# Kernel optimization log

Hardware: AMD Instinct MI355X
Metric: run time of the kernel (lower is better)

## Reference

```python
import jax, jax.numpy as jnp
import numpy as np

B, N, D = 4, 160, 64
ZI, ZE, L, LE = 64, 64, 4, 8
H1, H2 = 128, 64


def setup_inputs() -> dict:
    key = jax.random.key(0)
    ks = jax.random.split(key, 20)
    s = 0.05
    inp = {
        "node_embeddings": jax.random.normal(ks[0], (B, N, D), jnp.float32),
        "z_intra_t": jax.random.normal(ks[1], (B, ZI), jnp.float32),
        "z_inter_t": jax.random.normal(ks[2], (B, ZE), jnp.float32),
        # lag embedding table
        "lag_emb": jax.random.normal(ks[3], (L, LE), jnp.float32),
        # instantaneous reasoner: (2D+ZI)->128->64->1
        "Wi1": jax.random.normal(ks[4], (2 * D + ZI, H1), jnp.float32) * s,
        "bi1": jnp.zeros((H1,), jnp.float32),
        "Wi2": jax.random.normal(ks[5], (H1, H2), jnp.float32) * s,
        "bi2": jnp.zeros((H2,), jnp.float32),
        "Wi3": jax.random.normal(ks[6], (H2, 1), jnp.float32) * s,
        "bi3": jnp.zeros((1,), jnp.float32),
        # lagged reasoner: (2D+ZE+LE)->128->64->1
        "Wl1": jax.random.normal(ks[7], (2 * D + ZE + LE, H1), jnp.float32) * s,
        "bl1": jnp.zeros((H1,), jnp.float32),
        "Wl2": jax.random.normal(ks[8], (H1, H2), jnp.float32) * s,
        "bl2": jnp.zeros((H2,), jnp.float32),
        "Wl3": jax.random.normal(ks[9], (H2, 1), jnp.float32) * s,
        "bl3": jnp.zeros((1,), jnp.float32),
    }
    return inp


def reference(node_embeddings, z_intra_t, z_inter_t, lag_emb,
              Wi1, bi1, Wi2, bi2, Wi3, bi3,
              Wl1, bl1, Wl2, bl2, Wl3, bl3):
    # Instead of materializing concat([h_i, h_j, z, ...]) over N*N pairs,
    # split the first linear layer's weight along its input rows; the sum of
    # per-part projections equals the linear over the concatenation.
    ne = node_embeddings  # [B, N, D]

    # --- instantaneous reasoner ---
    Wi1_a, Wi1_b, Wi1_z = Wi1[:D], Wi1[D:2 * D], Wi1[2 * D:]
    pi = ne @ Wi1_a          # [B, N, H1] projection of h_i
    pj = ne @ Wi1_b          # [B, N, H1] projection of h_j
    pz = z_intra_t @ Wi1_z   # [B, H1]
    h = jax.nn.relu(pi[:, :, None, :] + pj[:, None, :, :]
                    + pz[:, None, None, :] + bi1)          # [B, N, N, H1]
    h = jax.nn.relu(h @ Wi2 + bi2)                         # [B, N, N, H2]
    W_logits = (h @ Wi3 + bi3)[..., 0]                     # [B, N, N]

    # --- lagged reasoner ---
    Wl1_a, Wl1_b = Wl1[:D], Wl1[D:2 * D]
    Wl1_z, Wl1_l = Wl1[2 * D:2 * D + ZE], Wl1[2 * D + ZE:]
    qi = ne @ Wl1_a          # [B, N, H1]
    qj = ne @ Wl1_b          # [B, N, H1]
    qz = z_inter_t @ Wl1_z   # [B, H1]
    ql = lag_emb @ Wl1_l     # [L, H1]
    g = jax.nn.relu(qi[:, None, :, None, :] + qj[:, None, None, :, :]
                    + qz[:, None, None, None, :] + ql[None, :, None, None, :]
                    + bl1)                                 # [B, L, N, N, H1]
    g = jax.nn.relu(g @ Wl2 + bl2)                         # [B, L, N, N, H2]
    A_logits = (g @ Wl3 + bl3)[..., 0]                     # [B, L, N, N]

    mask = 1.0 - jnp.eye(N, dtype=ne.dtype)
    W_t = jax.nn.sigmoid(W_logits) * mask
    A_lags_t = jax.nn.sigmoid(A_logits) * mask
    return (W_t, A_lags_t)
```

## Files before the change

### kernel.cpp

```cpp
#include <hip/hip_runtime.h>
#include <hip/hip_bf16.h>

#define B_   4
#define N_   160
#define D_   64
#define ZI_  64
#define H1_  128
#define H2_  64
#define L_   4
#define LE_  8

typedef __bf16 bf16x8 __attribute__((ext_vector_type(8)));
typedef float  f32x4  __attribute__((ext_vector_type(4)));
typedef unsigned int u32x4 __attribute__((ext_vector_type(4)));

static __device__ __forceinline__ unsigned pk_bf16(float a, float b) {
    __hip_bfloat162 h = __float22bfloat162_rn(float2{a, b});
    union { __hip_bfloat162 h; unsigned u; } c;
    c.h = h;
    return c.u;
}

__global__ __launch_bounds__(128) void stage_a(
    const float* __restrict__ ne,
    const float* __restrict__ zi,
    const float* __restrict__ ze,
    const float* __restrict__ lag,
    const float* __restrict__ Wi1,
    const float* __restrict__ bi1,
    const float* __restrict__ Wl1,
    const float* __restrict__ bl1,
    const float* __restrict__ Wi2,
    const float* __restrict__ bi2,
    const float* __restrict__ Wi3,
    const float* __restrict__ bi3,
    const float* __restrict__ Wl2,
    const float* __restrict__ bl2,
    const float* __restrict__ Wl3,
    const float* __restrict__ bl3,
    float* __restrict__ ui, float* __restrict__ uq,
    __bf16* __restrict__ vpi, __bf16* __restrict__ vpl,
    char* __restrict__ blob_i, char* __restrict__ blob_l)
{
    const int bi = blockIdx.x;
    const int b  = bi / N_;
    const int h  = threadIdx.x;

    const float* nerow = ne + bi * D_;

    float pi_ = 0.f, pj_ = 0.f, qi_ = 0.f, qj_ = 0.f;
#pragma unroll 16
    for (int d = 0; d < D_; ++d) {
        const float a = nerow[d];
        pi_ += a * Wi1[d * H1_ + h];
        pj_ += a * Wi1[(D_ + d) * H1_ + h];
        qi_ += a * Wl1[d * H1_ + h];
        qj_ += a * Wl1[(D_ + d) * H1_ + h];
    }
    float pz = 0.f, qz = 0.f;
#pragma unroll 16
    for (int z = 0; z < ZI_; ++z) {
        pz += zi[b * ZI_ + z] * Wi1[(2 * D_ + z) * H1_ + h];
        qz += ze[b * ZI_ + z] * Wl1[(2 * D_ + z) * H1_ + h];
    }

    ui[bi * H1_ + h] = pi_ + pz + bi1[h];

    const int hsw = (((h >> 3) ^ (bi & 7)) << 3) | (h & 7);
    vpi[bi * H1_ + hsw] = (__bf16)pj_;
    vpl[bi * H1_ + hsw] = (__bf16)qj_;

    const float qbase = qi_ + qz + bl1[h];
#pragma unroll
    for (int l = 0; l < L_; ++l) {
        float ql = 0.f;
#pragma unroll
        for (int e = 0; e < LE_; ++e)
            ql += lag[l * LE_ + e] * Wl1[(2 * D_ + ZI_ + e) * H1_ + h];
        uq[((b * L_ + l) * N_ + (bi % N_)) * H1_ + h] = qbase + ql;
    }

    if (bi < 2) {
        const float* Wsrc = (bi == 0) ? Wi2 : Wl2;
        char* blob = (bi == 0) ? blob_i : blob_l;
        __bf16* Wdst = (__bf16*)blob;
#pragma unroll
        for (int r = 0; r < 8; ++r) {
            const int fc = h + 128 * r;
            const int kt = fc >> 8, ct = (fc >> 6) & 3;
            const int q = (fc >> 4) & 3, c = fc & 15;
            bf16x8 t;
#pragma unroll
            for (int j = 0; j < 8; ++j)
                t[j] = (__bf16)Wsrc[(32 * kt + 8 * q + j) * H2_ + 16 * ct + c];
            *(bf16x8*)(Wdst + fc * 8) = t;
        }
        float* bdst = (float*)(blob + 16384);
        const float* b2s = (bi == 0) ? bi2 : bl2;
        const float* w3s = (bi == 0) ? Wi3 : Wl3;
        const float* b3s = (bi == 0) ? bi3 : bl3;
        if (h < H2_) bdst[h] = b2s[h];
        if (h < H2_) bdst[128 + h] = w3s[h];
        if (h == 0)  bdst[256] = b3s[0];
    }
}

__global__ __launch_bounds__(256, 3) void stage_b(
    const float* __restrict__ ui, const float* __restrict__ uq,
    const __bf16* __restrict__ vpi, const __bf16* __restrict__ vpl,
    const char* __restrict__ blob_i, const char* __restrict__ blob_l,
    float* __restrict__ out)
{
    __shared__ __align__(16) char lds[43008];
    __bf16* panel = (__bf16*)lds;
    char*   blob  = lds + 20480;
    float*  ulds  = (float*)(lds + 40960);

    const int t    = threadIdx.x;
    const int wid  = t >> 6;
    const int lane = t & 63;
    const int q = lane >> 4;
    const int c = lane & 15;

    const int blk    = blockIdx.x;
    const int rowgrp = blk >> 1;
    const int half   = blk & 1;
    const int wave   = rowgrp * 4 + wid;
    const int wave0  = rowgrp * 4;

    const __bf16* psrc;
    const char*   bsrc;
    const float*  usrc;
    if (rowgrp < 160) {
        psrc = vpi + (rowgrp / 40) * (N_ * H1_);
        bsrc = blob_i;
        usrc = ui + wave0 * H1_;
    } else {
        psrc = vpl + ((rowgrp - 160) / 160) * (N_ * H1_);
        bsrc = blob_l;
        usrc = uq + (wave0 - B_ * N_) * H1_;
    }
    psrc += 80 * half * H1_;

    {
        const char* gp = (const char*)psrc;
#pragma unroll
        for (int it = 0; it < 5; ++it)
            __builtin_amdgcn_global_load_lds(
                (const __attribute__((address_space(1))) void*)(gp + it * 4096 + t * 16),
                (__attribute__((address_space(3))) void*)(lds + it * 4096 + wid * 1024),
                16, 0, 0);
#pragma unroll
        for (int it = 0; it < 5; ++it)
            __builtin_amdgcn_global_load_lds(
                (const __attribute__((address_space(1))) void*)(bsrc + it * 4096 + t * 16),
                (__attribute__((address_space(3))) void*)(blob + it * 4096 + wid * 1024),
                16, 0, 0);
        if (wid < 2)
            __builtin_amdgcn_global_load_lds(
                (const __attribute__((address_space(1))) void*)((const char*)usrc + t * 16),
                (__attribute__((address_space(3))) void*)((char*)ulds + wid * 1024),
                16, 0, 0);
    }

    long obase;
    int  i;
    if (wave < B_ * N_) {
        i = wave % N_;
        obase = (long)wave * N_;
    } else {
        const int w2i = wave - B_ * N_;
        i = w2i % N_;
        obase = (long)B_ * N_ * N_ + (long)w2i * N_;
    }

    __syncthreads();

    bf16x8 bfr[4][4];
#pragma unroll
    for (int kt = 0; kt < 4; ++kt)
#pragma unroll
        for (int ct = 0; ct < 4; ++ct)
            bfr[kt][ct] = *(const bf16x8*)(blob + ((kt * 4 + ct) * 64 + lane) * 16);

    const float* bf32 = (const float*)(blob + 16384);
    float b2c[4], w3c[4];
#pragma unroll
    for (int ct = 0; ct < 4; ++ct) {
        b2c[ct] = bf32[16 * ct + c];
        w3c[ct] = bf32[128 + 16 * ct + c];
    }
    const float b3f = bf32[256];

    const float* ubase = ulds + wid * H1_;
    f32x4 ue[4], uo[4];
#pragma unroll
    for (int kt = 0; kt < 4; ++kt) {
        const f32x4 a0 = *(const f32x4*)(ubase + 32 * kt + 8 * q);
        const f32x4 a1 = *(const f32x4*)(ubase + 32 * kt + 8 * q + 4);
        ue[kt] = (f32x4){a0[0], a0[2], a1[0], a1[2]};
        uo[kt] = (f32x4){a0[1], a0[3], a1[1], a1[3]};
    }

    for (int jt = 0; jt < 5; ++jt) {
        const __bf16* prow = panel + (16 * jt + c) * H1_;
        f32x4 acc[4];
#pragma unroll
        for (int ct = 0; ct < 4; ++ct)
            acc[ct] = (f32x4){b2c[ct], b2c[ct], b2c[ct], b2c[ct]};

#pragma unroll
        for (int kt = 0; kt < 4; ++kt) {
            const u32x4 vw = *(const u32x4*)(prow + (((4 * kt + q) ^ (c & 7)) << 3));
            f32x4 vlo, vhi;
#pragma unroll
            for (int d = 0; d < 4; ++d) {
                vlo[d] = __uint_as_float(vw[d] << 16);
                vhi[d] = __uint_as_float(vw[d] & 0xffff0000u);
            }
            f32x4 xe = ue[kt] + vlo;
            f32x4 xo = uo[kt] + vhi;
            xe = __builtin_elementwise_max(xe, (f32x4)0.f);
            xo = __builtin_elementwise_max(xo, (f32x4)0.f);
            union { bf16x8 v; unsigned d[4]; } a;
#pragma unroll
            for (int d = 0; d < 4; ++d)
                a.d[d] = pk_bf16(xe[d], xo[d]);
#pragma unroll
            for (int ct = 0; ct < 4; ++ct)
                acc[ct] = __builtin_amdgcn_mfma_f32_16x16x32_bf16(
                    a.v, bfr[kt][ct], acc[ct], 0, 0, 0);
        }

        float logit[4];
#pragma unroll
        for (int r = 0; r < 4; ++r) {
            float p = 0.f;
#pragma unroll
            for (int ct = 0; ct < 4; ++ct)
                p += fmaxf(acc[ct][r], 0.f) * w3c[ct];
            p += __shfl_xor(p, 1);
            p += __shfl_xor(p, 2);
            p += __shfl_xor(p, 4);
            p += __shfl_xor(p, 8);
            logit[r] = p;
        }

        if (c < 4) {
            const int j = 80 * half + 16 * jt + 4 * q + c;
            const float lg = logit[c] + b3f;
            const float s = (j == i) ? 0.f : 1.f / (1.f + __expf(-lg));
            out[obase + j] = s;
        }
    }
}

extern "C" void kernel_launch(void* const* d_in, const int* in_sizes, int n_in,
                              void* d_out, int out_size, void* d_ws, size_t ws_size,
                              hipStream_t stream) {
    const float* ne  = (const float*)d_in[0];
    const float* zi  = (const float*)d_in[1];
    const float* ze  = (const float*)d_in[2];
    const float* lag = (const float*)d_in[3];
    const float* Wi1 = (const float*)d_in[4];
    const float* bi1 = (const float*)d_in[5];
    const float* Wi2 = (const float*)d_in[6];
    const float* bi2 = (const float*)d_in[7];
    const float* Wi3 = (const float*)d_in[8];
    const float* bi3 = (const float*)d_in[9];
    const float* Wl1 = (const float*)d_in[10];
    const float* bl1 = (const float*)d_in[11];
    const float* Wl2 = (const float*)d_in[12];
    const float* bl2 = (const float*)d_in[13];
    const float* Wl3 = (const float*)d_in[14];
    const float* bl3 = (const float*)d_in[15];

    float*  ws     = (float*)d_ws;
    float*  ui     = ws;
    float*  uqw    = ws + 81920;
    __bf16* vpi    = (__bf16*)(ws + 409600);
    __bf16* vpl    = vpi + 81920;
    char*   blob_i = (char*)d_ws + 1966080;
    char*   blob_l = blob_i + 20480;

    stage_a<<<B_ * N_, 128, 0, stream>>>(ne, zi, ze, lag, Wi1, bi1, Wl1, bl1,
                                         Wi2, bi2, Wi3, bi3, Wl2, bl2, Wl3, bl3,
                                         ui, uqw, vpi, vpl, blob_i, blob_l);

    stage_b<<<2 * (B_ * N_ + B_ * L_ * N_) / 4, 256, 0, stream>>>(
        ui, uqw, vpi, vpl, blob_i, blob_l,
        (float*)d_out);
}
```

Measured before the change: 111.1 us.

## Double block size to eight waves and stream weight fragments from LDS

Stage B now runs 512-thread blocks with eight rows per block, halving the grid and amortising each panel and weight-blob load over twice as many waves. The B-fragment registers and pre-split u vectors are dropped; weights are read from LDS inside the MFMA loop and u is read directly, using a permuted store layout from stage A so even and odd lanes land contiguously. The aim is lower register pressure and higher occupancy, paid for with more LDS reads per tile.

```diff
diff --git a/kernel.cpp b/kernel.cpp
--- a/kernel.cpp
+++ b/kernel.cpp
@@ -64,7 +64,10 @@
         qz += ze[b * ZI_ + z] * Wl1[(2 * D_ + z) * H1_ + h];
     }
 
-    ui[bi * H1_ + h] = pi_ + pz + bi1[h];
+    const int r7 = h & 7;
+    const int hp = (h & ~7) | ((r7 & 1) ? (4 + (r7 >> 1)) : (r7 >> 1));
+
+    ui[bi * H1_ + hp] = pi_ + pz + bi1[h];
 
     const int hsw = (((h >> 3) ^ (bi & 7)) << 3) | (h & 7);
     vpi[bi * H1_ + hsw] = (__bf16)pj_;
@@ -77,7 +80,7 @@
 #pragma unroll
         for (int e = 0; e < LE_; ++e)
             ql += lag[l * LE_ + e] * Wl1[(2 * D_ + ZI_ + e) * H1_ + h];
-        uq[((b * L_ + l) * N_ + (bi % N_)) * H1_ + h] = qbase + ql;
+        uq[((b * L_ + l) * N_ + (bi % N_)) * H1_ + hp] = qbase + ql;
     }
 
     if (bi < 2) {
@@ -105,13 +108,13 @@
     }
 }
 
-__global__ __launch_bounds__(256, 3) void stage_b(
+__global__ __launch_bounds__(512, 6) void stage_b(
     const float* __restrict__ ui, const float* __restrict__ uq,
     const __bf16* __restrict__ vpi, const __bf16* __restrict__ vpl,
     const char* __restrict__ blob_i, const char* __restrict__ blob_l,
     float* __restrict__ out)
 {
-    __shared__ __align__(16) char lds[43008];
+    __shared__ __align__(16) char lds[45056];
     __bf16* panel = (__bf16*)lds;
     char*   blob  = lds + 20480;
     float*  ulds  = (float*)(lds + 40960);
@@ -125,42 +128,32 @@
     const int blk    = blockIdx.x;
     const int rowgrp = blk >> 1;
     const int half   = blk & 1;
-    const int wave   = rowgrp * 4 + wid;
-    const int wave0  = rowgrp * 4;
+    const int wave   = rowgrp * 8 + wid;
+    const int row0   = rowgrp * 8;
 
     const __bf16* psrc;
     const char*   bsrc;
     const float*  usrc;
-    if (rowgrp < 160) {
-        psrc = vpi + (rowgrp / 40) * (N_ * H1_);
+    if (rowgrp < 80) {
+        psrc = vpi + (rowgrp / 20) * (N_ * H1_);
         bsrc = blob_i;
-        usrc = ui + wave0 * H1_;
+        usrc = ui + row0 * H1_;
     } else {
-        psrc = vpl + ((rowgrp - 160) / 160) * (N_ * H1_);
+        psrc = vpl + ((rowgrp - 80) / 80) * (N_ * H1_);
         bsrc = blob_l;
-        usrc = uq + (wave0 - B_ * N_) * H1_;
+        usrc = uq + (row0 - B_ * N_) * H1_;
     }
     psrc += 80 * half * H1_;
 
-    {
-        const char* gp = (const char*)psrc;
-#pragma unroll
-        for (int it = 0; it < 5; ++it)
-            __builtin_amdgcn_global_load_lds(
-                (const __attribute__((address_space(1))) void*)(gp + it * 4096 + t * 16),
-                (__attribute__((address_space(3))) void*)(lds + it * 4096 + wid * 1024),
-                16, 0, 0);
-#pragma unroll
-        for (int it = 0; it < 5; ++it)
-            __builtin_amdgcn_global_load_lds(
-                (const __attribute__((address_space(1))) void*)(bsrc + it * 4096 + t * 16),
-                (__attribute__((address_space(3))) void*)(blob + it * 4096 + wid * 1024),
-                16, 0, 0);
-        if (wid < 2)
-            __builtin_amdgcn_global_load_lds(
-                (const __attribute__((address_space(1))) void*)((const char*)usrc + t * 16),
-                (__attribute__((address_space(3))) void*)((char*)ulds + wid * 1024),
-                16, 0, 0);
+    for (int g = wid; g < 44; g += 8) {
+        const char* src;
+        if (g < 20)      src = (const char*)psrc + (g << 10);
+        else if (g < 40) src = bsrc + ((g - 20) << 10);
+        else             src = (const char*)usrc + ((g - 40) << 10);
+        __builtin_amdgcn_global_load_lds(
+            (const __attribute__((address_space(1))) void*)(src + lane * 16),
+            (__attribute__((address_space(3))) void*)(lds + (g << 10)),
+            16, 0, 0);
     }
 
     long obase;
@@ -176,13 +169,6 @@
 
     __syncthreads();
 
-    bf16x8 bfr[4][4];
-#pragma unroll
-    for (int kt = 0; kt < 4; ++kt)
-#pragma unroll
-        for (int ct = 0; ct < 4; ++ct)
-            bfr[kt][ct] = *(const bf16x8*)(blob + ((kt * 4 + ct) * 64 + lane) * 16);
-
     const float* bf32 = (const float*)(blob + 16384);
     float b2c[4], w3c[4];
 #pragma unroll
@@ -193,16 +179,9 @@
     const float b3f = bf32[256];
 
     const float* ubase = ulds + wid * H1_;
-    f32x4 ue[4], uo[4];
-#pragma unroll
-    for (int kt = 0; kt < 4; ++kt) {
-        const f32x4 a0 = *(const f32x4*)(ubase + 32 * kt + 8 * q);
-        const f32x4 a1 = *(const f32x4*)(ubase + 32 * kt + 8 * q + 4);
-        ue[kt] = (f32x4){a0[0], a0[2], a1[0], a1[2]};
-        uo[kt] = (f32x4){a0[1], a0[3], a1[1], a1[3]};
-    }
 
     for (int jt = 0; jt < 5; ++jt) {
+        asm volatile("" ::: "memory");
         const __bf16* prow = panel + (16 * jt + c) * H1_;
         f32x4 acc[4];
 #pragma unroll
@@ -212,24 +191,23 @@
 #pragma unroll
         for (int kt = 0; kt < 4; ++kt) {
             const u32x4 vw = *(const u32x4*)(prow + (((4 * kt + q) ^ (c & 7)) << 3));
-            f32x4 vlo, vhi;
+            const f32x4 ue = *(const f32x4*)(ubase + 32 * kt + 8 * q);
+            const f32x4 uo = *(const f32x4*)(ubase + 32 * kt + 8 * q + 4);
+            union { bf16x8 v; unsigned d[4]; } a;
 #pragma unroll
             for (int d = 0; d < 4; ++d) {
-                vlo[d] = __uint_as_float(vw[d] << 16);
-                vhi[d] = __uint_as_float(vw[d] & 0xffff0000u);
+                const unsigned w = vw[d];
+                const float lo = __uint_as_float(w << 16) + ue[d];
+                const float hi = __uint_as_float(w & 0xffff0000u) + uo[d];
+                a.d[d] = pk_bf16(fmaxf(lo, 0.f), fmaxf(hi, 0.f));
             }
-            f32x4 xe = ue[kt] + vlo;
-            f32x4 xo = uo[kt] + vhi;
-            xe = __builtin_elementwise_max(xe, (f32x4)0.f);
-            xo = __builtin_elementwise_max(xo, (f32x4)0.f);
-            union { bf16x8 v; unsigned d[4]; } a;
-#pragma unroll
-            for (int d = 0; d < 4; ++d)
-                a.d[d] = pk_bf16(xe[d], xo[d]);
-#pragma unroll
-            for (int ct = 0; ct < 4; ++ct)
+#pragma unroll
+            for (int ct = 0; ct < 4; ++ct) {
+                const bf16x8 bfrag =
+                    *(const bf16x8*)(blob + ((kt * 4 + ct) * 64 + lane) * 16);
                 acc[ct] = __builtin_amdgcn_mfma_f32_16x16x32_bf16(
-                    a.v, bfr[kt][ct], acc[ct], 0, 0, 0);
+                    a.v, bfrag, acc[ct], 0, 0, 0);
+            }
         }
 
         float logit[4];
@@ -287,7 +265,7 @@
                                          Wi2, bi2, Wi3, bi3, Wl2, bl2, Wl3, bl3,
                                          ui, uqw, vpi, vpl, blob_i, blob_l);
 
-    stage_b<<<2 * (B_ * N_ + B_ * L_ * N_) / 4, 256, 0, stream>>>(
+    stage_b<<<800, 512, 0, stream>>>(
         ui, uqw, vpi, vpl, blob_i, blob_l,
         (float*)d_out);
 }
```

Result: no change. 113.2 us (+2.0%).
